# Performance work log

Hardware: AMD Instinct MI355X
Metric: run time of the kernel (lower is better)

## Reference

```python
import jax, jax.numpy as jnp
import numpy as np

N_NODES = 50000
N_EDGES = 800000
NODE_DIM = 64
EDGE_DIM = 16
HIDDEN = 128
EPS = 1e-5


def _linear_init(key, fan_in, fan_out):
    k1, k2 = jax.random.split(key)
    bound = 1.0 / np.sqrt(fan_in)
    W = jax.random.uniform(k1, (fan_in, fan_out), minval=-bound, maxval=bound, dtype=jnp.float32)
    b = jax.random.uniform(k2, (fan_out,), minval=-bound, maxval=bound, dtype=jnp.float32)
    return W, b


def batchnorm(h, gamma, beta):
    # BatchNorm1d in training mode: batch mean/var (biased), eps=1e-5
    mu = jnp.mean(h, axis=0, keepdims=True)
    var = jnp.mean((h - mu) ** 2, axis=0, keepdims=True)
    return (h - mu) * jax.lax.rsqrt(var + EPS) * gamma + beta


def setup_inputs() -> dict:
    key = jax.random.key(0)
    ks = jax.random.split(key, 8)
    x = jax.random.normal(ks[0], (N_NODES, NODE_DIM), dtype=jnp.float32)
    edge_index = jax.random.randint(ks[1], (2, N_EDGES), 0, N_NODES, dtype=jnp.int64)
    edge_attr = jax.random.normal(ks[2], (N_EDGES, EDGE_DIM), dtype=jnp.float32)
    We1, be1 = _linear_init(ks[3], 2 * NODE_DIM + EDGE_DIM, HIDDEN)
    We2, be2 = _linear_init(ks[4], HIDDEN, HIDDEN)
    Wm, bm = _linear_init(ks[5], HIDDEN, HIDDEN)
    Wn1, bn1 = _linear_init(ks[6], NODE_DIM + HIDDEN, HIDDEN)
    Wn2, bn2 = _linear_init(ks[7], HIDDEN, HIDDEN)
    ones = jnp.ones((HIDDEN,), jnp.float32)
    zeros = jnp.zeros((HIDDEN,), jnp.float32)
    return dict(x=x, edge_index=edge_index, edge_attr=edge_attr,
                We1=We1, be1=be1, ge=ones, bbe=zeros, We2=We2, be2=be2,
                Wm=Wm, bm=bm,
                Wn1=Wn1, bn1=bn1, gn=ones, bbn=zeros, Wn2=Wn2, bn2=bn2)


def reference(x, edge_index, edge_attr, We1, be1, ge, bbe, We2, be2, Wm, bm, Wn1, bn1, gn, bbn, Wn2, bn2):
    row, col = edge_index[0], edge_index[1]
    # gather + concat -> edge network (Linear, BN, ReLU, Linear)
    edge_input = jnp.concatenate([x[row], x[col], edge_attr], axis=-1)  # [E, 2n+e]
    h = jax.nn.relu(batchnorm(edge_input @ We1 + be1, ge, bbe))
    edge_features = h @ We2 + be2
    # message MLP (Linear, ReLU)
    messages = jax.nn.relu(edge_features @ Wm + bm)  # [E, H]
    # scatter-add into source nodes
    agg = jax.ops.segment_sum(messages, row, num_segments=N_NODES)  # [N, H]
    # node network (Linear, BN, ReLU, Linear)
    node_input = jnp.concatenate([x, agg], axis=-1)
    hn = jax.nn.relu(batchnorm(node_input @ Wn1 + bn1, gn, bbn))
    return hn @ Wn2 + bn2
```

## Files before the change

kernel.cpp:

```cpp
#include <hip/hip_runtime.h>
#include <stdint.h>

#define NNODES 50000
#define NEDGES 800000
#define H 128
#define BN_EPS 1e-5f

typedef short short8 __attribute__((ext_vector_type(8)));
typedef short short4v __attribute__((ext_vector_type(4)));
typedef float f32x4 __attribute__((ext_vector_type(4)));

__device__ __forceinline__ float bf2f(unsigned short u) {
    unsigned int v = ((unsigned int)u) << 16;
    return __uint_as_float(v);
}
__device__ __forceinline__ unsigned short f2bf(float f) {
    unsigned int x = __float_as_uint(f);
    return (unsigned short)((x + 0x7FFFu + ((x >> 16) & 1u)) >> 16);
}
__device__ __forceinline__ short8 s8z() { short8 z = {0,0,0,0,0,0,0,0}; return z; }

template<int KB>
__device__ __forceinline__ void gemm_tile(const short* __restrict__ sA, const int SK,
                                          const unsigned short* __restrict__ WT, const int RK,
                                          const int n0, f32x4 acc[4][4], const int lane) {
    const int mr = lane & 15, quad = lane >> 4;
    const short* W = (const short*)WT;
    #pragma unroll
    for (int kb = 0; kb < KB; ++kb) {
        short8 a[4];
        #pragma unroll
        for (int mt = 0; mt < 4; ++mt)
            a[mt] = *(const short8*)&sA[(mt*16 + mr)*SK + kb*32 + quad*8];
        #pragma unroll
        for (int nt = 0; nt < 4; ++nt) {
            short8 b = *(const short8*)&W[(size_t)(n0 + nt*16 + mr)*RK + kb*32 + quad*8];
            #pragma unroll
            for (int mt = 0; mt < 4; ++mt)
                acc[mt][nt] = __builtin_amdgcn_mfma_f32_16x16x32_bf16(a[mt], b, acc[mt][nt], 0, 0, 0);
        }
    }
}

__global__ void k_fold(const float* __restrict__ We2, const float* __restrict__ be2,
                       const float* __restrict__ Wm, const float* __restrict__ bm,
                       float* __restrict__ W2m, float* __restrict__ b2m) {
    int j = threadIdx.x;
    int i = blockIdx.x;
    if (i < H) {
        float acc = 0.f;
        for (int k = 0; k < H; ++k) acc = fmaf(We2[i*H + k], Wm[k*H + j], acc);
        W2m[i*H + j] = acc;
    } else {
        float acc = bm[j];
        for (int k = 0; k < H; ++k) acc = fmaf(be2[k], Wm[k*H + j], acc);
        b2m[j] = acc;
    }
}

__global__ void k_prep2(const float* __restrict__ We1, const float* __restrict__ Wn1,
                        const float* __restrict__ Wn2,
                        unsigned short* __restrict__ WabT, unsigned short* __restrict__ Wn1T,
                        unsigned short* __restrict__ Wn2T, unsigned short* __restrict__ WcT,
                        int* __restrict__ cnt, float* __restrict__ S1f) {
    int i = blockIdx.x*256 + threadIdx.x;
    if (i < 16384) {
        int n = i >> 6, k = i & 63;
        WabT[n*64 + k] = f2bf(We1[(n < 128 ? k : 64 + k)*H + (n & 127)]);
    } else if (i < 40960) {
        int j = i - 16384; int n = j / 192, k = j - n*192;
        Wn1T[n*192 + k] = f2bf(Wn1[k*H + n]);
    } else if (i < 57344) {
        int j = i - 40960; int n = j >> 7, k = j & 127;
        Wn2T[n*H + k] = f2bf(Wn2[k*H + n]);
    } else if (i < 61440) {
        int j = i - 57344; int n = j >> 5, k = j & 31;
        WcT[n*32 + k] = (k < 16) ? f2bf(We1[(128 + k)*H + n]) : (unsigned short)0;
    } else if (i < 111440) {
        cnt[i - 61440] = 0;
    } else if (i < 112464) {
        S1f[i - 111440] = 0.f;
    }
}

__global__ void k_count(const int* __restrict__ ei, int* __restrict__ cnt) {
    int e = blockIdx.x*256 + threadIdx.x;
    if (e < NEDGES) atomicAdd(&cnt[ei[e]], 1);
}

__global__ void k_scanA(const int* __restrict__ cnt, int* __restrict__ bsum) {
    __shared__ int ws[4];
    const int tid = threadIdx.x;
    int i = blockIdx.x*256 + tid;
    int v = (i < NNODES) ? cnt[i] : 0;
    #pragma unroll
    for (int off = 32; off > 0; off >>= 1) v += __shfl_down(v, off);
    if ((tid & 63) == 0) ws[tid >> 6] = v;
    __syncthreads();
    if (tid == 0) bsum[blockIdx.x] = ws[0] + ws[1] + ws[2] + ws[3];
}

__global__ void k_scanB(const int* __restrict__ bsum, int* __restrict__ bpre,
                        int* __restrict__ offsets) {
    __shared__ int ws[4];
    const int tid = threadIdx.x;
    const int lane = tid & 63, wid = tid >> 6;
    int v = (tid < 196) ? bsum[tid] : 0;
    int xv = v;
    #pragma unroll
    for (int off = 1; off < 64; off <<= 1) {
        int y = __shfl_up(xv, off);
        if (lane >= off) xv += y;
    }
    if (lane == 63) ws[wid] = xv;
    __syncthreads();
    int base = 0;
    for (int w = 0; w < 4; ++w) if (w < wid) base += ws[w];
    int incl = base + xv;
    if (tid < 196) bpre[tid] = incl - v;
    if (tid == 255) offsets[NNODES] = incl;
}

__global__ void k_scanC(const int* __restrict__ cnt, const int* __restrict__ bpre,
                        int* __restrict__ offsets, int* __restrict__ cursor) {
    __shared__ int ws[4];
    const int tid = threadIdx.x;
    const int lane = tid & 63, wid = tid >> 6;
    int i = blockIdx.x*256 + tid;
    int v = (i < NNODES) ? cnt[i] : 0;
    int xv = v;
    #pragma unroll
    for (int off = 1; off < 64; off <<= 1) {
        int y = __shfl_up(xv, off);
        if (lane >= off) xv += y;
    }
    if (lane == 63) ws[wid] = xv;
    __syncthreads();
    int base = bpre[blockIdx.x];
    for (int w = 0; w < 4; ++w) if (w < wid) base += ws[w];
    int excl = base + xv - v;
    if (i < NNODES) { offsets[i] = excl; cursor[i] = excl; }
}

__global__ void k_scatter(const int* __restrict__ ei, int* __restrict__ cursor,
                          int* __restrict__ elist) {
    int e = blockIdx.x*256 + threadIdx.x;
    if (e < NEDGES) {
        int p = atomicAdd(&cursor[ei[e]], 1);
        elist[p] = e;
    }
}

__launch_bounds__(256)
__global__ void k_T(const float* __restrict__ x, const unsigned short* __restrict__ WabT,
                    unsigned short* __restrict__ T) {
    __shared__ short sA[128*72];
    const int tid = threadIdx.x;
    const int n0b = blockIdx.x*128;
    {
        const int rowl = tid >> 1, half = (tid & 1)*32;
        const int node = n0b + rowl;
        const bool ok = node < NNODES;
        #pragma unroll
        for (int c = 0; c < 4; ++c) {
            int k0 = half + c*8;
            short8 o = s8z();
            if (ok) {
                float4 a = *(const float4*)&x[node*64 + k0];
                float4 b = *(const float4*)&x[node*64 + k0 + 4];
                o[0]=(short)f2bf(a.x); o[1]=(short)f2bf(a.y); o[2]=(short)f2bf(a.z); o[3]=(short)f2bf(a.w);
                o[4]=(short)f2bf(b.x); o[5]=(short)f2bf(b.y); o[6]=(short)f2bf(b.z); o[7]=(short)f2bf(b.w);
            }
            *(short8*)&sA[rowl*72 + k0] = o;
        }
    }
    __syncthreads();
    const int wave = tid >> 6, lane = tid & 63;
    const int m0 = (wave & 1)*64;
    const int n0 = blockIdx.y*128 + (wave >> 1)*64;
    f32x4 acc[4][4];
    f32x4 z = {0.f, 0.f, 0.f, 0.f};
    #pragma unroll
    for (int mt = 0; mt < 4; ++mt)
        #pragma unroll
        for (int nt = 0; nt < 4; ++nt) acc[mt][nt] = z;
    gemm_tile<2>(sA + m0*72, 72, WabT, 64, n0, acc, lane);
    const int mr = lane & 15, quad = lane >> 4;
    #pragma unroll
    for (int nt = 0; nt < 4; ++nt) {
        int j = n0 + nt*16 + mr;
        #pragma unroll
        for (int mt = 0; mt < 4; ++mt) {
            int nb = n0b + m0 + mt*16 + quad*4;
            #pragma unroll
            for (int r = 0; r < 4; ++r) {
                int node = nb + r;
                if (node < NNODES) T[(size_t)node*256 + j] = f2bf(acc[mt][nt][r]);
            }
        }
    }
}

__launch_bounds__(256, 8)
__global__ void k_gather3(const unsigned short* __restrict__ T, const int* __restrict__ ei,
                          const int* __restrict__ elist, const float* __restrict__ ea,
                          const unsigned short* __restrict__ WcT, const float* __restrict__ be1,
                          unsigned short* __restrict__ hb,
                          float* __restrict__ gS, float* __restrict__ gSS) {
    __shared__ short sT[64*136];
    __shared__ float sS[H], sSS[H];
    const int tid = threadIdx.x;
    const int p0 = blockIdx.x*64;
    const int wave = tid >> 6, lane = tid & 63;
    const int mr = lane & 15, quad = lane >> 4;
    const int mbase = wave*16;
    if (tid < 128) { sS[tid] = 0.f; sSS[tid] = 0.f; }
    short8 a0 = s8z();
    if (quad < 2) {
        int e0i = elist[p0 + mbase + mr];
        f32x4 u0 = __builtin_nontemporal_load((const f32x4*)&ea[(size_t)e0i*16 + quad*8]);
        f32x4 u1 = __builtin_nontemporal_load((const f32x4*)&ea[(size_t)e0i*16 + quad*8 + 4]);
        a0[0]=(short)f2bf(u0[0]); a0[1]=(short)f2bf(u0[1]); a0[2]=(short)f2bf(u0[2]); a0[3]=(short)f2bf(u0[3]);
        a0[4]=(short)f2bf(u1[0]); a0[5]=(short)f2bf(u1[1]); a0[6]=(short)f2bf(u1[2]); a0[7]=(short)f2bf(u1[3]);
    }
    const int lp = tid >> 2, q4 = tid & 3;
    const int e = elist[p0 + lp];
    const int row = ei[e], col = ei[NEDGES + e];
    const unsigned short* Tr = &T[(size_t)row*256 + q4*32];
    const unsigned short* Tc = &T[(size_t)col*256 + 128 + q4*32];
    short8 t1[4], t2[4];
    #pragma unroll
    for (int c = 0; c < 4; ++c) {
        t1[c] = *(const short8*)&Tr[c*8];
        t2[c] = *(const short8*)&Tc[c*8];
    }
    #pragma unroll
    for (int c = 0; c < 4; ++c) {
        short8 o;
        #pragma unroll
        for (int i = 0; i < 8; ++i)
            o[i] = (short)f2bf(bf2f((unsigned short)t1[c][i]) + bf2f((unsigned short)t2[c][i]));
        *(short8*)&sT[lp*136 + q4*32 + c*8] = o;
    }
    f32x4 acc[8];
    f32x4 z = {0.f, 0.f, 0.f, 0.f};
    #pragma unroll
    for (int nt = 0; nt < 8; ++nt) acc[nt] = z;
    #pragma unroll
    for (int nt = 0; nt < 8; ++nt) {
        short8 b = *(const short8*)&WcT[(nt*16 + mr)*32 + quad*8];
        acc[nt] = __builtin_amdgcn_mfma_f32_16x16x32_bf16(a0, b, acc[nt], 0, 0, 0);
    }
    __syncthreads();
    #pragma unroll
    for (int nt = 0; nt < 8; ++nt) {
        int j = nt*16 + mr;
        float bia = be1[j];
        float s = 0.f, ssum = 0.f;
        #pragma unroll
        for (int r = 0; r < 4; ++r) {
            int m = mbase + quad*4 + r;
            float v = acc[nt][r] + bf2f((unsigned short)sT[m*136 + j]) + bia;
            sT[m*136 + j] = (short)f2bf(v);
            s += v; ssum += v*v;
        }
        s += __shfl_xor(s, 16);
        ssum += __shfl_xor(ssum, 16);
        s += __shfl_xor(s, 32);
        ssum += __shfl_xor(ssum, 32);
        if (quad == 0) {
            atomicAdd(&sS[j], s);
            atomicAdd(&sSS[j], ssum);
        }
    }
    __syncthreads();
    {
        const int sb = blockIdx.x >> 1;
        const int lpS = (blockIdx.x & 1)*64 + lp;
        #pragma unroll
        for (int c = 0; c < 4; ++c) {
            int k0 = q4*32 + c*8;
            short8 v = *(const short8*)&sT[lp*136 + k0];
            __builtin_nontemporal_store(v,
                (short8*)&hb[((size_t)(sb*16 + q4*4 + c)*128 + lpS)*8]);
        }
    }
    if (tid < 128) { atomicAdd(&gS[tid], sS[tid]); atomicAdd(&gSS[tid], sSS[tid]); }
}

__global__ void k_stats(const float* __restrict__ S, const float* __restrict__ SS,
                        const float* __restrict__ g, const float* __restrict__ b,
                        float invCount, float* __restrict__ scale, float* __restrict__ shift) {
    int j = threadIdx.x;
    float mu = S[j]*invCount;
    float var = SS[j]*invCount - mu*mu;
    float sc = rsqrtf(var + BN_EPS)*g[j];
    scale[j] = sc;
    shift[j] = b[j] - mu*sc;
}

__global__ void k_prep3(const float* __restrict__ W2m, const float* __restrict__ scale,
                        const float* __restrict__ shift, unsigned short* __restrict__ W2mST,
                        float* __restrict__ tvec, float* __restrict__ agg) {
    int i = blockIdx.x*256 + threadIdx.x;
    if (i < 16384) {
        int n = i >> 7, k = i & 127;
        W2mST[n*H + k] = f2bf(scale[k] * W2m[k*H + n]);
    } else if (i < 16512) {
        int k = i - 16384;
        tvec[k] = shift[k] / scale[k];
    } else if (i < 16512 + NNODES*H) {
        agg[i - 16512] = 0.f;
    }
}

__launch_bounds__(256)
__global__ void k_msgagg(const unsigned short* __restrict__ hb, const float* __restrict__ tvec,
                         const unsigned short* __restrict__ W2mST, const float* __restrict__ b2m,
                         const int* __restrict__ ei, const int* __restrict__ elist,
                         const int* __restrict__ offsets, float* __restrict__ agg) {
    __shared__ short sA[128*136];
    __shared__ int rows[128];
    __shared__ int segStart[130];
    __shared__ int wcnt[2];
    __shared__ int nsegS;
    const int tid = threadIdx.x;
    const int p0 = blockIdx.x*128;
    const int wave = tid >> 6, lane = tid & 63;
    const int mr = lane & 15, quad = lane >> 4;
    const int mbase = wave*32;
    short8 raw[4][2];
    #pragma unroll
    for (int kb = 0; kb < 4; ++kb)
        #pragma unroll
        for (int mt = 0; mt < 2; ++mt)
            raw[kb][mt] = __builtin_nontemporal_load(
                (const short8*)&hb[((size_t)(blockIdx.x*16 + kb*4 + quad)*128
                                    + mbase + mt*16 + mr)*8]);
    int pre = 0, st = 0;
    if (tid < 128) rows[tid] = ei[elist[p0 + tid]];
    __syncthreads();
    if (tid < 128) {
        int r0 = rows[tid];
        st = (tid == 0) || (rows[tid - 1] != r0);
        unsigned long long m = __ballot(st);
        int lane2 = tid & 63;
        pre = __popcll(m & ((1ull << lane2) - 1ull));
        if (lane2 == 63) wcnt[tid >> 6] = pre + st;
    }
    __syncthreads();
    if (tid < 128) {
        int base = (tid >= 64) ? wcnt[0] : 0;
        int sid = base + pre + st - 1;
        if (st) segStart[sid] = tid;
        if (tid == 127) {
            int ns = wcnt[0] + wcnt[1];
            nsegS = ns;
            segStart[ns] = 128;
        }
    }
    f32x4 acc[2][8];
    f32x4 z = {0.f, 0.f, 0.f, 0.f};
    #pragma unroll
    for (int mt = 0; mt < 2; ++mt)
        #pragma unroll
        for (int nt = 0; nt < 8; ++nt) acc[mt][nt] = z;
    #pragma unroll
    for (int kb = 0; kb < 4; ++kb) {
        float4 tq0 = *(const float4*)&tvec[kb*32 + quad*8];
        float4 tq1 = *(const float4*)&tvec[kb*32 + quad*8 + 4];
        short8 a[2];
        #pragma unroll
        for (int mt = 0; mt < 2; ++mt) {
            short8 rw = raw[kb][mt];
            short8 av;
            av[0] = (short)f2bf(fmaxf(bf2f((unsigned short)rw[0]) + tq0.x, 0.f));
            av[1] = (short)f2bf(fmaxf(bf2f((unsigned short)rw[1]) + tq0.y, 0.f));
            av[2] = (short)f2bf(fmaxf(bf2f((unsigned short)rw[2]) + tq0.z, 0.f));
            av[3] = (short)f2bf(fmaxf(bf2f((unsigned short)rw[3]) + tq0.w, 0.f));
            av[4] = (short)f2bf(fmaxf(bf2f((unsigned short)rw[4]) + tq1.x, 0.f));
            av[5] = (short)f2bf(fmaxf(bf2f((unsigned short)rw[5]) + tq1.y, 0.f));
            av[6] = (short)f2bf(fmaxf(bf2f((unsigned short)rw[6]) + tq1.z, 0.f));
            av[7] = (short)f2bf(fmaxf(bf2f((unsigned short)rw[7]) + tq1.w, 0.f));
            a[mt] = av;
        }
        #pragma unroll
        for (int nt = 0; nt < 8; ++nt) {
            short8 b = *(const short8*)&W2mST[(nt*16 + mr)*H + kb*32 + quad*8];
            acc[0][nt] = __builtin_amdgcn_mfma_f32_16x16x32_bf16(a[0], b, acc[0][nt], 0, 0, 0);
            acc[1][nt] = __builtin_amdgcn_mfma_f32_16x16x32_bf16(a[1], b, acc[1][nt], 0, 0, 0);
        }
    }
    #pragma unroll
    for (int nt = 0; nt < 8; ++nt) {
        int j = nt*16 + mr;
        float bias = b2m[j];
        #pragma unroll
        for (int mt = 0; mt < 2; ++mt) {
            #pragma unroll
            for (int r = 0; r < 4; ++r) {
                int m = mbase + mt*16 + quad*4 + r;
                sA[m*136 + j] = (short)f2bf(fmaxf(acc[mt][nt][r] + bias, 0.f));
            }
        }
    }
    __syncthreads();
    const int nseg = nsegS;
    for (int idx = tid; idx < (nseg << 5); idx += 256) {
        int s = idx >> 5, g = idx & 31;
        int j0 = g*4;
        int a0 = segStart[s], b0 = segStart[s + 1];
        float s0 = 0.f, s1 = 0.f, s2 = 0.f, s3 = 0.f;
        for (int i = a0; i < b0; ++i) {
            short4v v = *(const short4v*)&sA[i*136 + j0];
            s0 += bf2f((unsigned short)v[0]);
            s1 += bf2f((unsigned short)v[1]);
            s2 += bf2f((unsigned short)v[2]);
            s3 += bf2f((unsigned short)v[3]);
        }
        int r = rows[a0];
        bool interior = (a0 > 0) && (b0 < 128);
        bool full = interior || ((p0 + a0 == offsets[r]) && (p0 + b0 == offsets[r + 1]));
        float* dst = &agg[(size_t)r*H + j0];
        if (full) {
            f32x4 o = {s0, s1, s2, s3};
            *(f32x4*)dst = o;
        } else {
            atomicAdd(dst + 0, s0);
            atomicAdd(dst + 1, s1);
            atomicAdd(dst + 2, s2);
            atomicAdd(dst + 3, s3);
        }
    }
}

__launch_bounds__(256)
__global__ void k_node1(const float* __restrict__ x, const float* __restrict__ agg,
                        const unsigned short* __restrict__ Wn1T, const float* __restrict__ bn1,
                        float* __restrict__ h2, float* __restrict__ gS, float* __restrict__ gSS) {
    __shared__ short sA[128*200];
    __shared__ float sS[H], sSS[H];
    const int tid = threadIdx.x;
    if (tid < H) { sS[tid] = 0.f; sSS[tid] = 0.f; }
    const int n0b = blockIdx.x*128;
    {
        const int rowl = tid >> 1, half = (tid & 1)*96;
        const int node = n0b + rowl;
        const bool ok = node < NNODES;
        #pragma unroll
        for (int c = 0; c < 12; ++c) {
            int k0 = half + c*8;
            short8 o = s8z();
            if (ok) {
                float4 a, b;
                if (k0 < 64) {
                    a = *(const float4*)&x[node*64 + k0];
                    b = *(const float4*)&x[node*64 + k0 + 4];
                } else {
                    a = *(const float4*)&agg[(size_t)node*H + (k0 - 64)];
                    b = *(const float4*)&agg[(size_t)node*H + (k0 - 64) + 4];
                }
                o[0]=(short)f2bf(a.x); o[1]=(short)f2bf(a.y); o[2]=(short)f2bf(a.z); o[3]=(short)f2bf(a.w);
                o[4]=(short)f2bf(b.x); o[5]=(short)f2bf(b.y); o[6]=(short)f2bf(b.z); o[7]=(short)f2bf(b.w);
            }
            *(short8*)&sA[rowl*200 + k0] = o;
        }
    }
    __syncthreads();
    const int wave = tid >> 6, lane = tid & 63;
    const int m0 = (wave & 1)*64, n0 = (wave >> 1)*64;
    f32x4 acc[4][4];
    f32x4 z = {0.f, 0.f, 0.f, 0.f};
    #pragma unroll
    for (int mt = 0; mt < 4; ++mt)
        #pragma unroll
        for (int nt = 0; nt < 4; ++nt) acc[mt][nt] = z;
    gemm_tile<6>(sA + m0*200, 200, Wn1T, 192, n0, acc, lane);
    const int mr = lane & 15, quad = lane >> 4;
    #pragma unroll
    for (int nt = 0; nt < 4; ++nt) {
        int j = n0 + nt*16 + mr;
        float bias = bn1[j];
        float s = 0.f, ssum = 0.f;
        #pragma unroll
        for (int mt = 0; mt < 4; ++mt) {
            int nb = n0b + m0 + mt*16 + quad*4;
            #pragma unroll
            for (int r = 0; r < 4; ++r) {
                int node = nb + r;
                if (node < NNODES) {
                    float v = acc[mt][nt][r] + bias;
                    h2[(size_t)node*H + j] = v;
                    s += v; ssum += v*v;
                }
            }
        }
        atomicAdd(&sS[j], s);
        atomicAdd(&sSS[j], ssum);
    }
    __syncthreads();
    if (tid < H) { atomicAdd(&gS[tid], sS[tid]); atomicAdd(&gSS[tid], sSS[tid]); }
}

__launch_bounds__(256)
__global__ void k_node2(const float* __restrict__ h2, const float* __restrict__ scale,
                        const float* __restrict__ shift, const unsigned short* __restrict__ Wn2T,
                        const float* __restrict__ bn2, float* __restrict__ out) {
    __shared__ short sA[128*136];
    const int tid = threadIdx.x;
    const int n0b = blockIdx.x*128;
    {
        const int rowl = tid >> 1, half = (tid & 1)*64;
        const int node = n0b + rowl;
        const bool ok = node < NNODES;
        #pragma unroll
        for (int c = 0; c < 8; ++c) {
            int k0 = half + c*8;
            short8 o = s8z();
            if (ok) {
                float4 a = *(const float4*)&h2[(size_t)node*H + k0];
                float4 b = *(const float4*)&h2[(size_t)node*H + k0 + 4];
                float4 sc0 = *(const float4*)&scale[k0], sc1 = *(const float4*)&scale[k0 + 4];
                float4 sh0 = *(const float4*)&shift[k0], sh1 = *(const float4*)&shift[k0 + 4];
                o[0] = (short)f2bf(fmaxf(fmaf(a.x, sc0.x, sh0.x), 0.f));
                o[1] = (short)f2bf(fmaxf(fmaf(a.y, sc0.y, sh0.y), 0.f));
                o[2] = (short)f2bf(fmaxf(fmaf(a.z, sc0.z, sh0.z), 0.f));
                o[3] = (short)f2bf(fmaxf(fmaf(a.w, sc0.w, sh0.w), 0.f));
                o[4] = (short)f2bf(fmaxf(fmaf(b.x, sc1.x, sh1.x), 0.f));
                o[5] = (short)f2bf(fmaxf(fmaf(b.y, sc1.y, sh1.y), 0.f));
                o[6] = (short)f2bf(fmaxf(fmaf(b.z, sc1.z, sh1.z), 0.f));
                o[7] = (short)f2bf(fmaxf(fmaf(b.w, sc1.w, sh1.w), 0.f));
            }
            *(short8*)&sA[rowl*136 + k0] = o;
        }
    }
    __syncthreads();
    const int wave = tid >> 6, lane = tid & 63;
    const int m0 = (wave & 1)*64, n0 = (wave >> 1)*64;
    f32x4 acc[4][4];
    f32x4 z = {0.f, 0.f, 0.f, 0.f};
    #pragma unroll
    for (int mt = 0; mt < 4; ++mt)
        #pragma unroll
        for (int nt = 0; nt < 4; ++nt) acc[mt][nt] = z;
    gemm_tile<4>(sA + m0*136, 136, Wn2T, 128, n0, acc, lane);
    const int mr = lane & 15, quad = lane >> 4;
    #pragma unroll
    for (int nt = 0; nt < 4; ++nt) {
        int j = n0 + nt*16 + mr;
        float bias = bn2[j];
        #pragma unroll
        for (int mt = 0; mt < 4; ++mt) {
            int nb = n0b + m0 + mt*16 + quad*4;
            #pragma unroll
            for (int r = 0; r < 4; ++r) {
                int node = nb + r;
                if (node < NNODES) out[(size_t)node*H + j] = acc[mt][nt][r] + bias;
            }
        }
    }
}

extern "C" void kernel_launch(void* const* d_in, const int* in_sizes, int n_in,
                              void* d_out, int out_size, void* d_ws, size_t ws_size,
                              hipStream_t stream) {
    (void)in_sizes; (void)n_in; (void)out_size; (void)ws_size;
    const float* x   = (const float*)d_in[0];
    const int*   ei  = (const int*)d_in[1];
    const float* ea  = (const float*)d_in[2];
    const float* We1 = (const float*)d_in[3];
    const float* be1 = (const float*)d_in[4];
    const float* ge  = (const float*)d_in[5];
    const float* bbe = (const float*)d_in[6];
    const float* We2 = (const float*)d_in[7];
    const float* be2 = (const float*)d_in[8];
    const float* Wm  = (const float*)d_in[9];
    const float* bm  = (const float*)d_in[10];
    const float* Wn1 = (const float*)d_in[11];
    const float* bn1 = (const float*)d_in[12];
    const float* gn  = (const float*)d_in[13];
    const float* bbn = (const float*)d_in[14];
    const float* Wn2 = (const float*)d_in[15];
    const float* bn2 = (const float*)d_in[16];
    float* out = (float*)d_out;

    char* ws = (char*)d_ws;
    unsigned short* hb   = (unsigned short*)(ws);
    float*          h2   = (float*)(ws);
    float*          agg  = (float*)(ws + 204800000);
    unsigned short* Tbuf = (unsigned short*)(ws + 230400000);
    int* cnt     = (int*)(ws + 256000000);
    int* offsets = (int*)(ws + 256200192);
    int* cursor  = (int*)(ws + 256400448);
    int* bsum    = (int*)(ws + 256600448);
    int* bpre    = (int*)(ws + 256601472);
    int* elist   = (int*)(ws + 256602496);
    float* S1     = (float*)(ws + 259802496);
    float* SS1    = S1 + 128;
    float* S2     = S1 + 256;
    float* SS2    = S1 + 384;
    float* scale1 = S1 + 512;
    float* shift1 = S1 + 640;
    float* scale2 = S1 + 768;
    float* shift2 = S1 + 896;
    float* W2m  = (float*)(ws + 259806592);
    float* b2m  = (float*)(ws + 259872128);
    float* tvec = (float*)(ws + 259872640);
    unsigned short* WabT  = (unsigned short*)(ws + 259873152);
    unsigned short* Wn1T  = (unsigned short*)(ws + 259905920);
    unsigned short* Wn2T  = (unsigned short*)(ws + 259955072);
    unsigned short* W2mST = (unsigned short*)(ws + 259987840);
    unsigned short* WcT   = (unsigned short*)(ws + 260020608);

    k_fold<<<H + 1, H, 0, stream>>>(We2, be2, Wm, bm, W2m, b2m);
    k_prep2<<<440, 256, 0, stream>>>(We1, Wn1, Wn2, WabT, Wn1T, Wn2T, WcT, cnt, S1);
    k_count<<<NEDGES/256, 256, 0, stream>>>(ei, cnt);
    k_scanA<<<196, 256, 0, stream>>>(cnt, bsum);
    k_scanB<<<1, 256, 0, stream>>>(bsum, bpre, offsets);
    k_scanC<<<196, 256, 0, stream>>>(cnt, bpre, offsets, cursor);
    k_scatter<<<NEDGES/256, 256, 0, stream>>>(ei, cursor, elist);
    k_T<<<dim3(391, 2), 256, 0, stream>>>(x, WabT, Tbuf);
    k_gather3<<<NEDGES/64, 256, 0, stream>>>(Tbuf, ei, elist, ea, WcT, be1, hb, S1, SS1);
    k_stats<<<1, H, 0, stream>>>(S1, SS1, ge, bbe, 1.0f/NEDGES, scale1, shift1);
    k_prep3<<<12565, 256, 0, stream>>>(W2m, scale1, shift1, W2mST, tvec, agg);
    k_msgagg<<<NEDGES/128, 256, 0, stream>>>(hb, tvec, W2mST, b2m, ei, elist, offsets, agg);
    k_node1<<<391, 256, 0, stream>>>(x, agg, Wn1T, bn1, h2, S2, SS2);
    k_stats<<<1, H, 0, stream>>>(S2, SS2, gn, bbn, 1.0f/NNODES, scale2, shift2);
    k_node2<<<391, 256, 0, stream>>>(h2, scale2, shift2, Wn2T, bn2, out);
}
```

Measured before the change: 787.0 us.

## Widen gather and message kernels to 512-thread blocks, trim barriers

k_gather3 now processes 128 edges per 512-thread block. It issues the edge_attr loads early so they overlap the T gathers, and drops a barrier because each wave only touches the LDS rows it wrote itself. Per-column BN partial sums are kept in registers and reduced into LDS after a single barrier, and hb is stored in its native 128-row layout. k_msgagg goes to 512 threads, one 16-row M tile per wave instead of two, which cuts per-thread accumulators. The aim is better latency hiding and fewer syncs, at the risk of register caps from the tighter launch bounds and more block-level atomic traffic.

```diff
diff --git a/kernel.cpp b/kernel.cpp
--- a/kernel.cpp
+++ b/kernel.cpp
@@ -201,38 +201,41 @@
     }
 }
 
-__launch_bounds__(256, 8)
+__launch_bounds__(512, 8)
 __global__ void k_gather3(const unsigned short* __restrict__ T, const int* __restrict__ ei,
                           const int* __restrict__ elist, const float* __restrict__ ea,
                           const unsigned short* __restrict__ WcT, const float* __restrict__ be1,
                           unsigned short* __restrict__ hb,
                           float* __restrict__ gS, float* __restrict__ gSS) {
-    __shared__ short sT[64*136];
+    __shared__ short sT[128*136];
     __shared__ float sS[H], sSS[H];
     const int tid = threadIdx.x;
-    const int p0 = blockIdx.x*64;
+    const int p0 = blockIdx.x*128;
     const int wave = tid >> 6, lane = tid & 63;
     const int mr = lane & 15, quad = lane >> 4;
     const int mbase = wave*16;
-    if (tid < 128) { sS[tid] = 0.f; sSS[tid] = 0.f; }
-    short8 a0 = s8z();
-    if (quad < 2) {
-        int e0i = elist[p0 + mbase + mr];
-        f32x4 u0 = __builtin_nontemporal_load((const f32x4*)&ea[(size_t)e0i*16 + quad*8]);
-        f32x4 u1 = __builtin_nontemporal_load((const f32x4*)&ea[(size_t)e0i*16 + quad*8 + 4]);
-        a0[0]=(short)f2bf(u0[0]); a0[1]=(short)f2bf(u0[1]); a0[2]=(short)f2bf(u0[2]); a0[3]=(short)f2bf(u0[3]);
-        a0[4]=(short)f2bf(u1[0]); a0[5]=(short)f2bf(u1[1]); a0[6]=(short)f2bf(u1[2]); a0[7]=(short)f2bf(u1[3]);
-    }
     const int lp = tid >> 2, q4 = tid & 3;
+    const bool eaActive = (quad < 2);
     const int e = elist[p0 + lp];
+    int e0i = 0;
+    if (eaActive) e0i = elist[p0 + mbase + mr];
     const int row = ei[e], col = ei[NEDGES + e];
+    f32x4 u0, u1;
+    if (eaActive) {
+        u0 = __builtin_nontemporal_load((const f32x4*)&ea[(size_t)e0i*16 + quad*8]);
+        u1 = __builtin_nontemporal_load((const f32x4*)&ea[(size_t)e0i*16 + quad*8 + 4]);
+    }
     const unsigned short* Tr = &T[(size_t)row*256 + q4*32];
     const unsigned short* Tc = &T[(size_t)col*256 + 128 + q4*32];
     short8 t1[4], t2[4];
     #pragma unroll
-    for (int c = 0; c < 4; ++c) {
-        t1[c] = *(const short8*)&Tr[c*8];
-        t2[c] = *(const short8*)&Tc[c*8];
+    for (int c = 0; c < 4; ++c) t1[c] = *(const short8*)&Tr[c*8];
+    #pragma unroll
+    for (int c = 0; c < 4; ++c) t2[c] = *(const short8*)&Tc[c*8];
+    short8 a0 = s8z();
+    if (eaActive) {
+        a0[0]=(short)f2bf(u0[0]); a0[1]=(short)f2bf(u0[1]); a0[2]=(short)f2bf(u0[2]); a0[3]=(short)f2bf(u0[3]);
+        a0[4]=(short)f2bf(u1[0]); a0[5]=(short)f2bf(u1[1]); a0[6]=(short)f2bf(u1[2]); a0[7]=(short)f2bf(u1[3]);
     }
     #pragma unroll
     for (int c = 0; c < 4; ++c) {
@@ -251,7 +254,7 @@
         short8 b = *(const short8*)&WcT[(nt*16 + mr)*32 + quad*8];
         acc[nt] = __builtin_amdgcn_mfma_f32_16x16x32_bf16(a0, b, acc[nt], 0, 0, 0);
     }
-    __syncthreads();
+    float sAcc[8], ssAcc[8];
     #pragma unroll
     for (int nt = 0; nt < 8; ++nt) {
         int j = nt*16 + mr;
@@ -268,23 +271,26 @@
         ssum += __shfl_xor(ssum, 16);
         s += __shfl_xor(s, 32);
         ssum += __shfl_xor(ssum, 32);
-        if (quad == 0) {
-            atomicAdd(&sS[j], s);
-            atomicAdd(&sSS[j], ssum);
-        }
-    }
-    __syncthreads();
-    {
-        const int sb = blockIdx.x >> 1;
-        const int lpS = (blockIdx.x & 1)*64 + lp;
-        #pragma unroll
-        for (int c = 0; c < 4; ++c) {
-            int k0 = q4*32 + c*8;
-            short8 v = *(const short8*)&sT[lp*136 + k0];
-            __builtin_nontemporal_store(v,
-                (short8*)&hb[((size_t)(sb*16 + q4*4 + c)*128 + lpS)*8]);
-        }
-    }
+        sAcc[nt] = s;
+        ssAcc[nt] = ssum;
+    }
+    #pragma unroll
+    for (int c = 0; c < 4; ++c) {
+        int k0 = q4*32 + c*8;
+        short8 v = *(const short8*)&sT[lp*136 + k0];
+        __builtin_nontemporal_store(v,
+            (short8*)&hb[((size_t)(blockIdx.x*16 + q4*4 + c)*128 + lp)*8]);
+    }
+    if (tid < 128) { sS[tid] = 0.f; sSS[tid] = 0.f; }
+    __syncthreads();
+    if (quad == 0) {
+        #pragma unroll
+        for (int nt = 0; nt < 8; ++nt) {
+            atomicAdd(&sS[nt*16 + mr], sAcc[nt]);
+            atomicAdd(&sSS[nt*16 + mr], ssAcc[nt]);
+        }
+    }
+    __syncthreads();
     if (tid < 128) { atomicAdd(&gS[tid], sS[tid]); atomicAdd(&gSS[tid], sSS[tid]); }
 }
 
@@ -314,7 +320,7 @@
     }
 }
 
-__launch_bounds__(256)
+__launch_bounds__(512, 8)
 __global__ void k_msgagg(const unsigned short* __restrict__ hb, const float* __restrict__ tvec,
                          const unsigned short* __restrict__ W2mST, const float* __restrict__ b2m,
                          const int* __restrict__ ei, const int* __restrict__ elist,
@@ -328,15 +334,13 @@
     const int p0 = blockIdx.x*128;
     const int wave = tid >> 6, lane = tid & 63;
     const int mr = lane & 15, quad = lane >> 4;
-    const int mbase = wave*32;
-    short8 raw[4][2];
+    const int mbase = wave*16;
+    short8 raw[4];
     #pragma unroll
     for (int kb = 0; kb < 4; ++kb)
-        #pragma unroll
-        for (int mt = 0; mt < 2; ++mt)
-            raw[kb][mt] = __builtin_nontemporal_load(
-                (const short8*)&hb[((size_t)(blockIdx.x*16 + kb*4 + quad)*128
-                                    + mbase + mt*16 + mr)*8]);
+        raw[kb] = __builtin_nontemporal_load(
+            (const short8*)&hb[((size_t)(blockIdx.x*16 + kb*4 + quad)*128
+                                + mbase + mr)*8]);
     int pre = 0, st = 0;
     if (tid < 128) rows[tid] = ei[elist[p0 + tid]];
     __syncthreads();
@@ -359,36 +363,28 @@
             segStart[ns] = 128;
         }
     }
-    f32x4 acc[2][8];
+    f32x4 acc[8];
     f32x4 z = {0.f, 0.f, 0.f, 0.f};
     #pragma unroll
-    for (int mt = 0; mt < 2; ++mt)
-        #pragma unroll
-        for (int nt = 0; nt < 8; ++nt) acc[mt][nt] = z;
+    for (int nt = 0; nt < 8; ++nt) acc[nt] = z;
     #pragma unroll
     for (int kb = 0; kb < 4; ++kb) {
         float4 tq0 = *(const float4*)&tvec[kb*32 + quad*8];
         float4 tq1 = *(const float4*)&tvec[kb*32 + quad*8 + 4];
-        short8 a[2];
-        #pragma unroll
-        for (int mt = 0; mt < 2; ++mt) {
-            short8 rw = raw[kb][mt];
-            short8 av;
-            av[0] = (short)f2bf(fmaxf(bf2f((unsigned short)rw[0]) + tq0.x, 0.f));
-            av[1] = (short)f2bf(fmaxf(bf2f((unsigned short)rw[1]) + tq0.y, 0.f));
-            av[2] = (short)f2bf(fmaxf(bf2f((unsigned short)rw[2]) + tq0.z, 0.f));
-            av[3] = (short)f2bf(fmaxf(bf2f((unsigned short)rw[3]) + tq0.w, 0.f));
-            av[4] = (short)f2bf(fmaxf(bf2f((unsigned short)rw[4]) + tq1.x, 0.f));
-            av[5] = (short)f2bf(fmaxf(bf2f((unsigned short)rw[5]) + tq1.y, 0.f));
-            av[6] = (short)f2bf(fmaxf(bf2f((unsigned short)rw[6]) + tq1.z, 0.f));
-            av[7] = (short)f2bf(fmaxf(bf2f((unsigned short)rw[7]) + tq1.w, 0.f));
-            a[mt] = av;
-        }
+        short8 rw = raw[kb];
+        short8 av;
+        av[0] = (short)f2bf(fmaxf(bf2f((unsigned short)rw[0]) + tq0.x, 0.f));
+        av[1] = (short)f2bf(fmaxf(bf2f((unsigned short)rw[1]) + tq0.y, 0.f));
+        av[2] = (short)f2bf(fmaxf(bf2f((unsigned short)rw[2]) + tq0.z, 0.f));
+        av[3] = (short)f2bf(fmaxf(bf2f((unsigned short)rw[3]) + tq0.w, 0.f));
+        av[4] = (short)f2bf(fmaxf(bf2f((unsigned short)rw[4]) + tq1.x, 0.f));
+        av[5] = (short)f2bf(fmaxf(bf2f((unsigned short)rw[5]) + tq1.y, 0.f));
+        av[6] = (short)f2bf(fmaxf(bf2f((unsigned short)rw[6]) + tq1.z, 0.f));
+        av[7] = (short)f2bf(fmaxf(bf2f((unsigned short)rw[7]) + tq1.w, 0.f));
         #pragma unroll
         for (int nt = 0; nt < 8; ++nt) {
             short8 b = *(const short8*)&W2mST[(nt*16 + mr)*H + kb*32 + quad*8];
-            acc[0][nt] = __builtin_amdgcn_mfma_f32_16x16x32_bf16(a[0], b, acc[0][nt], 0, 0, 0);
-            acc[1][nt] = __builtin_amdgcn_mfma_f32_16x16x32_bf16(a[1], b, acc[1][nt], 0, 0, 0);
+            acc[nt] = __builtin_amdgcn_mfma_f32_16x16x32_bf16(av, b, acc[nt], 0, 0, 0);
         }
     }
     #pragma unroll
@@ -396,17 +392,14 @@
         int j = nt*16 + mr;
         float bias = b2m[j];
         #pragma unroll
-        for (int mt = 0; mt < 2; ++mt) {
-            #pragma unroll
-            for (int r = 0; r < 4; ++r) {
-                int m = mbase + mt*16 + quad*4 + r;
-                sA[m*136 + j] = (short)f2bf(fmaxf(acc[mt][nt][r] + bias, 0.f));
-            }
+        for (int r = 0; r < 4; ++r) {
+            int m = mbase + quad*4 + r;
+            sA[m*136 + j] = (short)f2bf(fmaxf(acc[nt][r] + bias, 0.f));
         }
     }
     __syncthreads();
     const int nseg = nsegS;
-    for (int idx = tid; idx < (nseg << 5); idx += 256) {
+    for (int idx = tid; idx < (nseg << 5); idx += 512) {
         int s = idx >> 5, g = idx & 31;
         int j0 = g*4;
         int a0 = segStart[s], b0 = segStart[s + 1];
@@ -620,10 +613,10 @@
     k_scanC<<<196, 256, 0, stream>>>(cnt, bpre, offsets, cursor);
     k_scatter<<<NEDGES/256, 256, 0, stream>>>(ei, cursor, elist);
     k_T<<<dim3(391, 2), 256, 0, stream>>>(x, WabT, Tbuf);
-    k_gather3<<<NEDGES/64, 256, 0, stream>>>(Tbuf, ei, elist, ea, WcT, be1, hb, S1, SS1);
+    k_gather3<<<NEDGES/128, 512, 0, stream>>>(Tbuf, ei, elist, ea, WcT, be1, hb, S1, SS1);
     k_stats<<<1, H, 0, stream>>>(S1, SS1, ge, bbe, 1.0f/NEDGES, scale1, shift1);
     k_prep3<<<12565, 256, 0, stream>>>(W2m, scale1, shift1, W2mST, tvec, agg);
-    k_msgagg<<<NEDGES/128, 256, 0, stream>>>(hb, tvec, W2mST, b2m, ei, elist, offsets, agg);
+    k_msgagg<<<NEDGES/128, 512, 0, stream>>>(hb, tvec, W2mST, b2m, ei, elist, offsets, agg);
     k_node1<<<391, 256, 0, stream>>>(x, agg, Wn1T, bn1, h2, S2, SS2);
     k_stats<<<1, H, 0, stream>>>(S2, SS2, gn, bbn, 1.0f/NNODES, scale2, shift2);
     k_node2<<<391, 256, 0, stream>>>(h2, scale2, shift2, Wn2T, bn2, out);
```

New measurement: 772.0 us. About the same (-1.9%).
